# Kernel optimization log

Measured on AMD Instinct MI355X. Metric: run time of the kernel, lower is better.

## Reference

```python
import jax, jax.numpy as jnp
from jax import lax
import numpy as np

B = 32          # batch
E = 768         # embedding_dim == hidden_dim (required for the module to run)
V = 8192        # vocabulary_size
MAX_LEN = 256   # max_seq_length


def setup_inputs() -> dict:
    key = jax.random.key(0)
    ks = jax.random.split(key, 10)
    s = 0.02
    return {
        "latent": jax.random.normal(ks[0], (B, E), jnp.float32),
        "W_lat": jax.random.normal(ks[1], (E, E), jnp.float32) * s,
        "b_lat": jnp.zeros((E,), jnp.float32),
        "emb":   jax.random.normal(ks[2], (V, E), jnp.float32) * s,
        "W_ih":  jax.random.normal(ks[3], (3 * E, E), jnp.float32) * s,
        "W_hh":  jax.random.normal(ks[4], (3 * E, E), jnp.float32) * s,
        "b_ih":  jnp.zeros((3 * E,), jnp.float32),
        "b_hh":  jnp.zeros((3 * E,), jnp.float32),
        "W_out": jax.random.normal(ks[5], (V, E), jnp.float32) * s,
        "b_out": jnp.zeros((V,), jnp.float32),
    }


def reference(latent, W_lat, b_lat, emb, W_ih, W_hh, b_ih, b_hh, W_out, b_out):
    # initial hidden state: projected latent, shape [B, E]
    h0 = latent @ W_lat.T + b_lat
    # decoder starts from token id 1 (<sos>)
    tok0 = jnp.ones((latent.shape[0],), jnp.int32)

    def step(carry, _):
        h, tok = carry
        x = emb[tok]                                  # [B, E] embedding lookup
        gi = x @ W_ih.T + b_ih                        # [B, 3E]
        gh = h @ W_hh.T + b_hh                        # [B, 3E]
        i_r, i_z, i_n = jnp.split(gi, 3, axis=-1)
        h_r, h_z, h_n = jnp.split(gh, 3, axis=-1)
        r = jax.nn.sigmoid(i_r + h_r)
        z = jax.nn.sigmoid(i_z + h_z)
        n = jnp.tanh(i_n + r * h_n)
        h_new = (1.0 - z) * n + z * h                 # torch GRU cell update
        pred = h_new @ W_out.T + b_out                # [B, V]
        tok_new = jnp.argmax(pred, axis=-1).astype(jnp.int32)  # greedy decode
        return (h_new, tok_new), pred

    _, preds = lax.scan(step, (h0, tok0), None, length=MAX_LEN)  # [T, B, V]
    return preds.transpose(1, 0, 2)                               # [B, T, V]
```

## Files before the change

kernel.cpp:

```cpp
#include <hip/hip_runtime.h>
#include <stdint.h>


typedef unsigned long long u64;
typedef unsigned int u32;
typedef _Float16 f16;
using half8 = __attribute__((ext_vector_type(8))) _Float16;
using f32x4 = __attribute__((ext_vector_type(4))) float;
using uint4v = __attribute__((ext_vector_type(4))) unsigned int;

#define E_ 768
#define V_ 8192
#define T_ 256
#define HP 24576
#define IH_PLANE (2304*768)
#define OUT_PLANE (8192*768)
#define NBLK 256

#define AGENT_LD(p)    __hip_atomic_load((p), __ATOMIC_RELAXED, __HIP_MEMORY_SCOPE_AGENT)
#define AGENT_ST(p,v)  __hip_atomic_store((p), (v), __ATOMIC_RELAXED, __HIP_MEMORY_SCOPE_AGENT)
#define AGENT_ADD(p,v) __hip_atomic_fetch_add((p), (v), __ATOMIC_RELAXED, __HIP_MEMORY_SCOPE_AGENT)

__device__ __forceinline__ f32x4 mfma16(half8 a, half8 b, f32x4 c){
  return __builtin_amdgcn_mfma_f32_16x16x32_f16(a, b, c, 0, 0, 0);
}
__device__ __forceinline__ void split2(float f, f16& hi, f16& lo){
  f16 h = (f16)f; hi = h; lo = (f16)((f - (float)h) * 4096.0f);
}
__device__ __forceinline__ u32 packh(float f){
  f16 h, l; split2(f, h, l);
  return (u32)__builtin_bit_cast(unsigned short, h) |
         ((u32)__builtin_bit_cast(unsigned short, l) << 16);
}
__device__ __forceinline__ u64 packkey(float f, int v){
  u32 fb = __float_as_uint(f);
  u32 s  = fb ^ ((u32)((int32_t)fb>>31) | 0x80000000u);
  return ((u64)s<<32) | (u64)(0xFFFFFFFFu - (u32)v);
}

#define NB_CONV 1200
#define NB_H0   96
#define NG_IH   221184
#define NG_ALL  1228800

__global__ __launch_bounds__(256) void prep_k(
    const float* __restrict__ W_ih, const float* __restrict__ W_hh, const float* __restrict__ W_out,
    const float* __restrict__ latent, const float* __restrict__ W_lat, const float* __restrict__ b_lat,
    f16* __restrict__ Wih_s, f16* __restrict__ Whh_s, f16* __restrict__ Wout_s,
    float* __restrict__ h_f32, u32* __restrict__ h_pack, unsigned* __restrict__ bar)
{
  int blk = blockIdx.x;
  if (blk < NB_CONV){
    for (int g = blk*256 + threadIdx.x; g < NG_ALL; g += NB_CONV*256){
      const float* src; f16* hi; f16* lo; int off;
      if (g < NG_IH)        { src=W_ih; hi=Wih_s; lo=Wih_s+IH_PLANE; off=g*8; }
      else if (g < 2*NG_IH) { src=W_hh; hi=Whh_s; lo=Whh_s+IH_PLANE; off=(g-NG_IH)*8; }
      else                  { src=W_out; hi=Wout_s; lo=Wout_s+OUT_PLANE; off=(g-2*NG_IH)*8; }
      float4 a = *(const float4*)(src+off);
      float4 b = *(const float4*)(src+off+4);
      float fs[8] = {a.x,a.y,a.z,a.w,b.x,b.y,b.z,b.w};
      half8 vh, vl;
      #pragma unroll
      for (int j=0;j<8;j++){ f16 h,l; split2(fs[j],h,l); vh[j]=h; vl[j]=l; }
      *(half8*)(hi+off) = vh;
      *(half8*)(lo+off) = vl;
    }
  } else {
    if (blk==NB_CONV) bar[threadIdx.x] = 0;
    int tid = (blk-NB_CONV)*256 + threadIdx.x;
    int b = tid/768, e = tid - b*768;
    const float4* wr = (const float4*)(W_lat + (size_t)e*768);
    const float4* xr = (const float4*)(latent + (size_t)b*768);
    float s0=0.f,s1=0.f,s2=0.f,s3=0.f;
    for (int k=0;k<192;k++){
      float4 w = wr[k]; float4 x = xr[k];
      s0 += w.x*x.x; s1 += w.y*x.y; s2 += w.z*x.z; s3 += w.w*x.w;
    }
    float acc = b_lat[e] + ((s0+s1)+(s2+s3));
    h_f32[b*768+e] = acc;
    h_pack[b*768+e] = packh(acc);
  }
}

__global__ __launch_bounds__(512) void gitab_k(
    const float* __restrict__ emb, const f16* __restrict__ Wih_s, float* __restrict__ gi_tab)
{
  __shared__ float red[3][8][2][64][4];
  const int bid = blockIdx.x, tid = threadIdx.x;
  const int tb = bid>>1, half = bid&1;
  const int w = tid>>6, lane = tid&63, col = lane&15, kg = lane>>4, kc = w;
  half8 ah[2][3], al[2][3];
  #pragma unroll
  for (int m=0;m<2;m++)
    #pragma unroll
    for (int i=0;i<3;i++){
      const float* src = emb + (size_t)(tb*32 + m*16 + col)*768 + kc*96 + i*32 + kg*8;
      float4 x0 = *(const float4*)src, x1 = *(const float4*)(src+4);
      float fs[8] = {x0.x,x0.y,x0.z,x0.w,x1.x,x1.y,x1.z,x1.w};
      half8 vh, vl;
      #pragma unroll
      for (int j=0;j<8;j++){ f16 h,l; split2(fs[j],h,l); vh[j]=h; vl[j]=l; }
      ah[m][i]=vh; al[m][i]=vl;
    }
  for (int g=0; g<24; ++g){
    #pragma unroll
    for (int j=0;j<3;j++){
      const int nt = half*72 + g*3 + j;
      f32x4 a0[2], a1[2];
      #pragma unroll
      for (int m=0;m<2;m++){ a0[m]=f32x4{0,0,0,0}; a1[m]=f32x4{0,0,0,0}; }
      #pragma unroll
      for (int i=0;i<3;i++){
        size_t o = (size_t)(nt*16+col)*768 + kc*96 + i*32 + kg*8;
        half8 bh = *(const half8*)(Wih_s + o);
        half8 bl = *(const half8*)(Wih_s + IH_PLANE + o);
        #pragma unroll
        for (int m=0;m<2;m++){
          a0[m] = mfma16(ah[m][i], bh, a0[m]);
          a1[m] = mfma16(ah[m][i], bl, a1[m]);
          a1[m] = mfma16(al[m][i], bh, a1[m]);
        }
      }
      #pragma unroll
      for (int m=0;m<2;m++){
        f32x4 v;
        #pragma unroll
        for (int r=0;r<4;r++) v[r] = a0[m][r] + a1[m][r]*(1.0f/4096.0f);
        *(f32x4*)&red[j][w][m][lane][0] = v;
      }
    }
    __syncthreads();
    if (w < 6){
      const int j = w>>1, m = w&1;
      f32x4 s = {0,0,0,0};
      #pragma unroll
      for (int ww=0; ww<8; ww++) s += *(const f32x4*)&red[j][ww][m][lane][0];
      const int nt = half*72 + g*3 + j;
      const int tokr = tb*32 + m*16 + kg*4;
      #pragma unroll
      for (int r=0;r<4;r++)
        gi_tab[(size_t)(tokr+r)*2304 + nt*16 + col] = s[r];
    }
    __syncthreads();
  }
}

__device__ __forceinline__ void gridbar(unsigned* bar, unsigned target){
  __syncthreads();
  if (threadIdx.x == 0){
    const int g = blockIdx.x & 7;
    unsigned old = AGENT_ADD(&bar[g*16], 1u);
    if (old == 32u*target - 1u)
      AGENT_ADD(&bar[128], 1u);
    int spins = 0;
    while (AGENT_LD(&bar[128]) < 8u*target){
      __builtin_amdgcn_s_sleep(1);
      if ((++spins & 2047) == 0)
        AGENT_ADD(&bar[128], 0u);
    }
  }
  __syncthreads();
}

__global__ __launch_bounds__(512, 2) void decode_k(
    const f16* __restrict__ Wout_s, const f16* __restrict__ Whh_s, const float* __restrict__ gi_tab,
    float* __restrict__ gh_buf, const float* __restrict__ h_f32, u32* __restrict__ h_pack,
    u64* __restrict__ candbuf, const float* __restrict__ b_ih, const float* __restrict__ b_hh,
    const float* __restrict__ b_out, float* __restrict__ out, unsigned* __restrict__ bar)
{
  __shared__ float red[3][8][2][64][4];
  __shared__ u64 amkey[32];
  const int bid = blockIdx.x, tid = threadIdx.x;
  const int w = tid>>6, lane = tid&63, col = lane&15, kg = lane>>4, kc = w;

  const f16* srcH[3] = {Wout_s, Wout_s, (bid<144)? Whh_s : Wout_s};
  const f16* srcL[3] = {Wout_s+OUT_PLANE, Wout_s+OUT_PLANE,
                        (bid<144)? Whh_s+IH_PLANE : Wout_s+OUT_PLANE};
  const int  rowb[3] = {bid*16, 4096+bid*16, (bid<144)? bid*16 : 0};
  half8 bf_h[3][3], bf_l[3][3];
  #pragma unroll
  for (int s=0;s<3;s++)
    #pragma unroll
    for (int i=0;i<3;i++){
      size_t o = (size_t)(rowb[s]+col)*768 + kc*96 + i*32 + kg*8;
      bf_h[s][i] = *(const half8*)(srcH[s] + o);
      bf_l[s][i] = *(const half8*)(srcL[s] + o);
    }
  float bo_reg[2];
  bo_reg[0] = b_out[bid*16 + col];
  bo_reg[1] = b_out[4096 + bid*16 + col];

  int cb = 0, ce = 0; float hreg = 0.f;
  float bir=0,biz=0,bin_=0,bhr=0,bhz=0,bhn=0;
  if (bid < 48){
    int gid = bid*512 + tid;
    cb = gid/768; ce = gid - cb*768;
    hreg = h_f32[cb*768 + ce];
    bir=b_ih[ce]; biz=b_ih[768+ce]; bin_=b_ih[1536+ce];
    bhr=b_hh[ce]; bhz=b_hh[768+ce]; bhn=b_hh[1536+ce];
  }

  unsigned bt = 0;
  for (int t=0; t<=256; ++t){
    if (tid < 32) amkey[tid] = 0;
    uint4v qa[2][3], qb[2][3];
    #pragma unroll
    for (int m=0;m<2;m++)
      #pragma unroll
      for (int i=0;i<3;i++){
        const u32* hp = h_pack + (m*16+col)*768 + kc*96 + i*32 + kg*8;
        asm volatile("global_load_dwordx4 %0, %1, off sc0 sc1"
                     : "=&v"(qa[m][i]) : "v"(hp));
        asm volatile("global_load_dwordx4 %0, %1, off offset:16 sc0 sc1"
                     : "=&v"(qb[m][i]) : "v"(hp));
      }
    asm volatile("s_waitcnt vmcnt(0)" ::: "memory");
    __builtin_amdgcn_sched_barrier(0);
    half8 ah[2][3], al[2][3];
    #pragma unroll
    for (int m=0;m<2;m++)
      #pragma unroll
      for (int i=0;i<3;i++){
        uint4v wh, wl;
        u32 d[8] = {qa[m][i][0],qa[m][i][1],qa[m][i][2],qa[m][i][3],
                    qb[m][i][0],qb[m][i][1],qb[m][i][2],qb[m][i][3]};
        #pragma unroll
        for (int j=0;j<4;j++){
          u32 w0 = d[2*j], w1 = d[2*j+1];
          wh[j] = (w0 & 0xffffu) | (w1 << 16);
          wl[j] = (w0 >> 16) | (w1 & 0xffff0000u);
        }
        ah[m][i] = __builtin_bit_cast(half8, wh);
        al[m][i] = __builtin_bit_cast(half8, wl);
      }
    #pragma unroll
    for (int s=0;s<3;s++){
      f32x4 a0[2], a1[2];
      #pragma unroll
      for (int m=0;m<2;m++){ a0[m]=f32x4{0,0,0,0}; a1[m]=f32x4{0,0,0,0}; }
      #pragma unroll
      for (int i=0;i<3;i++)
        #pragma unroll
        for (int m=0;m<2;m++){
          a0[m] = mfma16(ah[m][i], bf_h[s][i], a0[m]);
          a1[m] = mfma16(ah[m][i], bf_l[s][i], a1[m]);
          a1[m] = mfma16(al[m][i], bf_h[s][i], a1[m]);
        }
      #pragma unroll
      for (int m=0;m<2;m++){
        f32x4 v;
        #pragma unroll
        for (int r=0;r<4;r++) v[r] = a0[m][r] + a1[m][r]*(1.0f/4096.0f);
        *(f32x4*)&red[s][w][m][lane][0] = v;
      }
    }
    __syncthreads();
    float sv[2][4];
    bool have_out = false;
    if (w < 3){
      const int s = w;
      float vm[2][4];
      #pragma unroll
      for (int m=0;m<2;m++){
        f32x4 sum = {0,0,0,0};
        #pragma unroll
        for (int ww=0; ww<8; ww++) sum += *(const f32x4*)&red[s][ww][m][lane][0];
        #pragma unroll
        for (int r=0;r<4;r++) vm[m][r] = sum[r];
      }
      if (s < 2){
        if (t >= 1){
          have_out = true;
          const int v = s*4096 + bid*16 + col;
          const float bo = bo_reg[s];
          #pragma unroll
          for (int m=0;m<2;m++)
            #pragma unroll
            for (int r=0;r<4;r++){
              const int b = m*16 + kg*4 + r;
              const float p = vm[m][r] + bo;
              sv[m][r] = p;
              u64 key = packkey(p, v);
              #pragma unroll
              for (int off=1; off<16; off<<=1){
                u64 o = __shfl_xor((unsigned long long)key, off);
                if (o > key) key = o;
              }
              if (col == 0) atomicMax(&amkey[b], key);
            }
        }
      } else if (bid < 144){
        const int gr = bid*16 + col;
        #pragma unroll
        for (int m=0;m<2;m++)
          #pragma unroll
          for (int r=0;r<4;r++)
            AGENT_ST(&gh_buf[(m*16+kg*4+r)*2304 + gr], vm[m][r]);
      }
    }
    __syncthreads();
    if (t >= 1 && tid < 32) AGENT_ST(&candbuf[(size_t)bid*32 + tid], amkey[tid]);
    if (have_out){
      const int v = w*4096 + bid*16 + col;
      #pragma unroll
      for (int m=0;m<2;m++)
        #pragma unroll
        for (int r=0;r<4;r++)
          out[(size_t)(m*16+kg*4+r)*((size_t)T_*V_) + (size_t)(t-1)*V_ + v] = sv[m][r];
    }
    if (t == 256) break;
    gridbar(bar, ++bt);
    if (bid < 48){
      int tok = 1;
      if (t > 0){
        u64 k = 0;
        #pragma unroll
        for (int j=0;j<4;j++){
          u64 c = AGENT_LD(&candbuf[(size_t)(lane + 64*j)*32 + cb]);
          if (c > k) k = c;
        }
        #pragma unroll
        for (int off=1; off<64; off<<=1){
          u64 o = __shfl_xor((unsigned long long)k, off);
          if (o > k) k = o;
        }
        tok = (int)(0xFFFFFFFFu - (unsigned)(k & 0xFFFFFFFFull));
      }
      const float* gp = gi_tab + (size_t)tok*2304 + ce;
      const float gir = gp[0]    + bir;
      const float giz = gp[768]  + biz;
      const float gin = gp[1536] + bin_;
      float* hb = gh_buf + cb*2304 + ce;
      const float ghr = AGENT_LD(hb)        + bhr;
      const float ghz = AGENT_LD(hb + 768)  + bhz;
      const float ghn = AGENT_LD(hb + 1536) + bhn;
      const float rr = 1.0f/(1.0f+expf(-(gir+ghr)));
      const float zz = 1.0f/(1.0f+expf(-(giz+ghz)));
      const float nn = tanhf(gin + rr*ghn);
      hreg = (1.0f-zz)*nn + zz*hreg;
      AGENT_ST(&h_pack[cb*768 + ce], packh(hreg));
    }
    gridbar(bar, ++bt);
  }
}

extern "C" void kernel_launch(void* const* d_in, const int* in_sizes, int n_in,
                              void* d_out, int out_size, void* d_ws, size_t ws_size,
                              hipStream_t stream){
  const float* latent = (const float*)d_in[0];
  const float* W_lat  = (const float*)d_in[1];
  const float* b_lat  = (const float*)d_in[2];
  const float* emb    = (const float*)d_in[3];
  const float* W_ih   = (const float*)d_in[4];
  const float* W_hh   = (const float*)d_in[5];
  const float* b_ih   = (const float*)d_in[6];
  const float* b_hh   = (const float*)d_in[7];
  const float* W_out  = (const float*)d_in[8];
  const float* b_out  = (const float*)d_in[9];
  float* out = (float*)d_out;
  (void)in_sizes; (void)n_in; (void)out_size; (void)ws_size;

  char* ws = (char*)d_ws;
  size_t off = 0;
  auto carve = [&](size_t bytes)->char*{
    char* p = ws + off; off += (bytes + 255) & ~(size_t)255; return p;
  };
  f16*      Wih_s  = (f16*)     carve((size_t)2*IH_PLANE*2);
  f16*      Whh_s  = (f16*)     carve((size_t)2*IH_PLANE*2);
  f16*      Wout_s = (f16*)     carve((size_t)2*OUT_PLANE*2);
  float*    gi_tab = (float*)   carve((size_t)8192*2304*4);
  float*    gh_buf = (float*)   carve((size_t)32*2304*4);
  float*    h_f32  = (float*)   carve((size_t)HP*4);
  u32*      h_pack = (u32*)     carve((size_t)HP*4);
  u64*      candbuf= (u64*)     carve((size_t)256*32*8);
  unsigned* bar    = (unsigned*)carve(2048);

  hipLaunchKernelGGL(prep_k, dim3(NB_CONV+NB_H0), dim3(256), 0, stream,
                     W_ih, W_hh, W_out, latent, W_lat, b_lat,
                     Wih_s, Whh_s, Wout_s, h_f32, h_pack, bar);
  hipLaunchKernelGGL(gitab_k, dim3(512), dim3(512), 0, stream, emb, Wih_s, gi_tab);

  void* kargs[] = {
    (void*)&Wout_s, (void*)&Whh_s, (void*)&gi_tab, (void*)&gh_buf, (void*)&h_f32,
    (void*)&h_pack, (void*)&candbuf, (void*)&b_ih, (void*)&b_hh, (void*)&b_out,
    (void*)&out, (void*)&bar
  };
  (void)hipLaunchCooperativeKernel((void*)decode_k, dim3(NBLK), dim3(512), kargs, 0, stream);
}
```

Baseline: 3.366 ms.

## Version hidden state per step, move logit stores after barrier, compact gi table

The single h_pack buffer becomes a per-timestep h_seq array. Each step reads a fresh address, so the cache-bypassing inline-asm loads and explicit waitcnt are replaced by plain vector loads. The output logit stores move from before the grid barrier to after it, so they overlap with the GRU update phase instead of delaying barrier arrival. The candidate buffer is transposed so each batch row's 256 candidates sit contiguously for the argmax read, and the gi table is stored as packed fp16 hi/lo pairs. The cost is more workspace for the h history, plus the risk that relying on fresh addresses for coherence without sc bits is unsafe.

```diff
diff --git a/kernel.cpp b/kernel.cpp
--- a/kernel.cpp
+++ b/kernel.cpp
@@ -32,6 +32,11 @@
   return (u32)__builtin_bit_cast(unsigned short, h) |
          ((u32)__builtin_bit_cast(unsigned short, l) << 16);
 }
+__device__ __forceinline__ float unpackh(u32 u){
+  f16 h = __builtin_bit_cast(f16, (unsigned short)(u & 0xffffu));
+  f16 l = __builtin_bit_cast(f16, (unsigned short)(u >> 16));
+  return (float)h + (float)l * (1.0f/4096.0f);
+}
 __device__ __forceinline__ u64 packkey(float f, int v){
   u32 fb = __float_as_uint(f);
   u32 s  = fb ^ ((u32)((int32_t)fb>>31) | 0x80000000u);
@@ -47,7 +52,7 @@
     const float* __restrict__ W_ih, const float* __restrict__ W_hh, const float* __restrict__ W_out,
     const float* __restrict__ latent, const float* __restrict__ W_lat, const float* __restrict__ b_lat,
     f16* __restrict__ Wih_s, f16* __restrict__ Whh_s, f16* __restrict__ Wout_s,
-    float* __restrict__ h_f32, u32* __restrict__ h_pack, unsigned* __restrict__ bar)
+    float* __restrict__ h_f32, u32* __restrict__ h_seq, unsigned* __restrict__ bar)
 {
   int blk = blockIdx.x;
   if (blk < NB_CONV){
@@ -78,12 +83,12 @@
     }
     float acc = b_lat[e] + ((s0+s1)+(s2+s3));
     h_f32[b*768+e] = acc;
-    h_pack[b*768+e] = packh(acc);
+    h_seq[b*768+e] = packh(acc);
   }
 }
 
 __global__ __launch_bounds__(512) void gitab_k(
-    const float* __restrict__ emb, const f16* __restrict__ Wih_s, float* __restrict__ gi_tab)
+    const float* __restrict__ emb, const f16* __restrict__ Wih_s, u32* __restrict__ gi_tab)
 {
   __shared__ float red[3][8][2][64][4];
   const int bid = blockIdx.x, tid = threadIdx.x;
@@ -139,7 +144,7 @@
       const int tokr = tb*32 + m*16 + kg*4;
       #pragma unroll
       for (int r=0;r<4;r++)
-        gi_tab[(size_t)(tokr+r)*2304 + nt*16 + col] = s[r];
+        gi_tab[(size_t)(tokr+r)*2304 + nt*16 + col] = packh(s[r]);
     }
     __syncthreads();
   }
@@ -163,15 +168,18 @@
 }
 
 __global__ __launch_bounds__(512, 2) void decode_k(
-    const f16* __restrict__ Wout_s, const f16* __restrict__ Whh_s, const float* __restrict__ gi_tab,
-    float* __restrict__ gh_buf, const float* __restrict__ h_f32, u32* __restrict__ h_pack,
-    u64* __restrict__ candbuf, const float* __restrict__ b_ih, const float* __restrict__ b_hh,
+    const f16* __restrict__ Wout_s, const f16* __restrict__ Whh_s, const u32* __restrict__ gi_tab,
+    float* __restrict__ gh_buf, const float* __restrict__ h_f32, u32* __restrict__ h_seq,
+    u64* __restrict__ candbufT, const float* __restrict__ b_ih, const float* __restrict__ b_hh,
     const float* __restrict__ b_out, float* __restrict__ out, unsigned* __restrict__ bar)
 {
   __shared__ float red[3][8][2][64][4];
   __shared__ u64 amkey[32];
   const int bid = blockIdx.x, tid = threadIdx.x;
   const int w = tid>>6, lane = tid&63, col = lane&15, kg = lane>>4, kc = w;
+
+  __builtin_amdgcn_fence(__ATOMIC_ACQUIRE, "agent");
+  __syncthreads();
 
   const f16* srcH[3] = {Wout_s, Wout_s, (bid<144)? Whh_s : Wout_s};
   const f16* srcL[3] = {Wout_s+OUT_PLANE, Wout_s+OUT_PLANE,
@@ -203,19 +211,16 @@
   unsigned bt = 0;
   for (int t=0; t<=256; ++t){
     if (tid < 32) amkey[tid] = 0;
+    const u32* hbase = h_seq + (size_t)t*HP;
     uint4v qa[2][3], qb[2][3];
     #pragma unroll
     for (int m=0;m<2;m++)
       #pragma unroll
       for (int i=0;i<3;i++){
-        const u32* hp = h_pack + (m*16+col)*768 + kc*96 + i*32 + kg*8;
-        asm volatile("global_load_dwordx4 %0, %1, off sc0 sc1"
-                     : "=&v"(qa[m][i]) : "v"(hp));
-        asm volatile("global_load_dwordx4 %0, %1, off offset:16 sc0 sc1"
-                     : "=&v"(qb[m][i]) : "v"(hp));
-      }
-    asm volatile("s_waitcnt vmcnt(0)" ::: "memory");
-    __builtin_amdgcn_sched_barrier(0);
+        const uint4v* hp = (const uint4v*)(hbase + (m*16+col)*768 + kc*96 + i*32 + kg*8);
+        qa[m][i] = hp[0];
+        qb[m][i] = hp[1];
+      }
     half8 ah[2][3], al[2][3];
     #pragma unroll
     for (int m=0;m<2;m++)
@@ -299,24 +304,35 @@
       }
     }
     __syncthreads();
-    if (t >= 1 && tid < 32) AGENT_ST(&candbuf[(size_t)bid*32 + tid], amkey[tid]);
-    if (have_out){
-      const int v = w*4096 + bid*16 + col;
-      #pragma unroll
-      for (int m=0;m<2;m++)
-        #pragma unroll
-        for (int r=0;r<4;r++)
-          out[(size_t)(m*16+kg*4+r)*((size_t)T_*V_) + (size_t)(t-1)*V_ + v] = sv[m][r];
-    }
-    if (t == 256) break;
+    if (t >= 1 && tid < 32) AGENT_ST(&candbufT[(size_t)tid*256 + bid], amkey[tid]);
+    if (t == 256){
+      if (have_out){
+        const int v = w*4096 + bid*16 + col;
+        #pragma unroll
+        for (int m=0;m<2;m++)
+          #pragma unroll
+          for (int r=0;r<4;r++)
+            out[(size_t)(m*16+kg*4+r)*((size_t)T_*V_) + (size_t)(t-1)*V_ + v] = sv[m][r];
+      }
+      break;
+    }
     gridbar(bar, ++bt);
-    if (bid < 48){
+    if (bid >= 48){
+      if (have_out){
+        const int v = w*4096 + bid*16 + col;
+        #pragma unroll
+        for (int m=0;m<2;m++)
+          #pragma unroll
+          for (int r=0;r<4;r++)
+            out[(size_t)(m*16+kg*4+r)*((size_t)T_*V_) + (size_t)(t-1)*V_ + v] = sv[m][r];
+      }
+    } else {
       int tok = 1;
       if (t > 0){
         u64 k = 0;
         #pragma unroll
         for (int j=0;j<4;j++){
-          u64 c = AGENT_LD(&candbuf[(size_t)(lane + 64*j)*32 + cb]);
+          u64 c = AGENT_LD(&candbufT[(size_t)cb*256 + lane + 64*j]);
           if (c > k) k = c;
         }
         #pragma unroll
@@ -326,10 +342,10 @@
         }
         tok = (int)(0xFFFFFFFFu - (unsigned)(k & 0xFFFFFFFFull));
       }
-      const float* gp = gi_tab + (size_t)tok*2304 + ce;
-      const float gir = gp[0]    + bir;
-      const float giz = gp[768]  + biz;
-      const float gin = gp[1536] + bin_;
+      const u32* gp = gi_tab + (size_t)tok*2304 + ce;
+      const float gir = unpackh(gp[0])    + bir;
+      const float giz = unpackh(gp[768])  + biz;
+      const float gin = unpackh(gp[1536]) + bin_;
       float* hb = gh_buf + cb*2304 + ce;
       const float ghr = AGENT_LD(hb)        + bhr;
       const float ghz = AGENT_LD(hb + 768)  + bhz;
@@ -338,7 +354,15 @@
       const float zz = 1.0f/(1.0f+expf(-(giz+ghz)));
       const float nn = tanhf(gin + rr*ghn);
       hreg = (1.0f-zz)*nn + zz*hreg;
-      AGENT_ST(&h_pack[cb*768 + ce], packh(hreg));
+      AGENT_ST(&h_seq[(size_t)(t+1)*HP + cb*768 + ce], packh(hreg));
+      if (have_out){
+        const int v = w*4096 + bid*16 + col;
+        #pragma unroll
+        for (int m=0;m<2;m++)
+          #pragma unroll
+          for (int r=0;r<4;r++)
+            out[(size_t)(m*16+kg*4+r)*((size_t)T_*V_) + (size_t)(t-1)*V_ + v] = sv[m][r];
+      }
     }
     gridbar(bar, ++bt);
   }
@@ -368,21 +392,21 @@
   f16*      Wih_s  = (f16*)     carve((size_t)2*IH_PLANE*2);
   f16*      Whh_s  = (f16*)     carve((size_t)2*IH_PLANE*2);
   f16*      Wout_s = (f16*)     carve((size_t)2*OUT_PLANE*2);
-  float*    gi_tab = (float*)   carve((size_t)8192*2304*4);
+  u32*      gi_tab = (u32*)     carve((size_t)8192*2304*4);
   float*    gh_buf = (float*)   carve((size_t)32*2304*4);
   float*    h_f32  = (float*)   carve((size_t)HP*4);
-  u32*      h_pack = (u32*)     carve((size_t)HP*4);
-  u64*      candbuf= (u64*)     carve((size_t)256*32*8);
+  u32*      h_seq  = (u32*)     carve((size_t)257*HP*4);
+  u64*      candbufT=(u64*)     carve((size_t)32*256*8);
   unsigned* bar    = (unsigned*)carve(2048);
 
   hipLaunchKernelGGL(prep_k, dim3(NB_CONV+NB_H0), dim3(256), 0, stream,
                      W_ih, W_hh, W_out, latent, W_lat, b_lat,
-                     Wih_s, Whh_s, Wout_s, h_f32, h_pack, bar);
+                     Wih_s, Whh_s, Wout_s, h_f32, h_seq, bar);
   hipLaunchKernelGGL(gitab_k, dim3(512), dim3(512), 0, stream, emb, Wih_s, gi_tab);
 
   void* kargs[] = {
     (void*)&Wout_s, (void*)&Whh_s, (void*)&gi_tab, (void*)&gh_buf, (void*)&h_f32,
-    (void*)&h_pack, (void*)&candbuf, (void*)&b_ih, (void*)&b_hh, (void*)&b_out,
+    (void*)&h_seq, (void*)&candbufT, (void*)&b_ih, (void*)&b_hh, (void*)&b_out,
     (void*)&out, (void*)&bar
   };
   (void)hipLaunchCooperativeKernel((void*)decode_k, dim3(NBLK), dim3(512), kargs, 0, stream);
```

Measured after the change: 3.083 ms. -8.4%, faster.
